# Performance work log

Measured on AMD Instinct MI355X. Metric: run time of the kernel, lower is better.

Reference implementation:

```python
import jax, jax.numpy as jnp
import numpy as np
from jax.scipy.special import logsumexp

ALPHA = 1.0
TOP_K = 128
SK_EPS = 0.001   # sinkhorn entropic epsilon
SK_ITERS = 20    # max_iter (thresh early-exit dropped for jit; 20 fixed iters)
CLIP_MIN = 0.0001


def _cdist(x, y):
    # batched Euclidean distance, safe-sqrt so grad at 0 is 0 (matches torch.cdist subgradient)
    d2 = (jnp.sum(x * x, -1)[..., :, None] + jnp.sum(y * y, -1)[..., None, :]
          - 2.0 * jnp.einsum('bnd,bmd->bnm', x, y))
    d2 = jnp.maximum(d2, 0.0)
    safe = jnp.where(d2 > 0, d2, 1.0)
    return jnp.where(d2 > 0, jnp.sqrt(safe), 0.0)


def _sinkhorn(cost, p, q):
    # log-domain entropic OT with marginals p [B,N], q [B,M]
    logp, logq = jnp.log(p), jnp.log(q)

    def M(u, v):
        return (-cost + u[..., :, None] + v[..., None, :]) / SK_EPS

    def body(carry, _):
        u, v = carry
        u = SK_EPS * (logp - logsumexp(M(u, v), axis=-1)) + u
        v = SK_EPS * (logq - logsumexp(M(u, v), axis=-2)) + v
        return (u, v), None

    u0 = jnp.zeros_like(p)
    v0 = jnp.zeros_like(q)
    (u, v), _ = jax.lax.scan(body, (u0, v0), None, length=SK_ITERS)
    return jnp.exp(M(u, v))  # transport plan gamma [B,N,M]


def setup_inputs() -> dict:
    key = jax.random.key(0)
    ks = jax.random.split(key, 6)
    B, N, M, D = 8, 2048, 2048, 256
    return {
        'src': jax.random.normal(ks[0], (B, N, 3), dtype=jnp.float32),
        'tgt': jax.random.normal(ks[1], (B, M, 3), dtype=jnp.float32),
        'src_feats': jax.random.normal(ks[2], (B, N, D), dtype=jnp.float32),
        'tgt_feats': jax.random.uniform(ks[3], (B, M, D), dtype=jnp.float32),
        'src_o': jax.random.uniform(ks[4], (B, N), dtype=jnp.float32),
        'tgt_o': jax.random.uniform(ks[5], (B, M), dtype=jnp.float32),
    }


def reference(src, tgt, src_feats, tgt_feats, src_o, tgt_o):
    src_pi = src_o / jnp.maximum(jnp.sum(src_o, -1, keepdims=True), CLIP_MIN)
    tgt_pi = tgt_o / jnp.maximum(jnp.sum(tgt_o, -1, keepdims=True), CLIP_MIN)
    cost = _cdist(src_feats, tgt_feats)                       # [B,N,M]
    gamma = _sinkhorn(cost, src_pi, tgt_pi)                   # [B,N,M]
    src_corr = (jnp.einsum('bnm,bmd->bnd', gamma, tgt)
                / jnp.maximum(jnp.sum(gamma, -1, keepdims=True), CLIP_MIN))
    prob = jnp.max(gamma, axis=-1)                            # [B,N]
    _, idx = jax.lax.top_k(prob, TOP_K)                       # [B,K]
    src_k = jnp.take_along_axis(src, idx[:, :, None], axis=1)       # [B,K,3]
    tgt_k = jnp.take_along_axis(src_corr, idx[:, :, None], axis=1)  # [B,K,3]
    alpha2 = ALPHA * ALPHA
    src_edge = _cdist(src_k, src_k)
    tgt_edge = _cdist(tgt_k, tgt_k)
    z = jnp.abs(src_edge - tgt_edge)
    loss = jnp.sum(1.0 - jnp.exp(-0.5 * z * z / alpha2), axis=-1)
    return jnp.mean(loss)
```

## Files before the change

kernel.cpp:

```cpp
#include <hip/hip_runtime.h>
#include <math.h>

#define Bb 8
#define Nn 2048
#define Mm 2048
#define Dd 256
#define TOPK 128
#define SK_ITERS 20
#define RB 8
#define NEG_INIT (-1e30f)
#define SCALE_L2 (-1442.6950408889634f)

__device__ __forceinline__ void lse_merge(float& m, float& s, float m2, float s2) {
    float d = m2 - m;
    float e = exp2f(-fabsf(d));
    bool up = (d > 0.f);
    s = up ? fmaf(s, e, s2) : fmaf(s2, e, s);
    m = up ? m2 : m;
}

__global__ void wl_init_kernel(const float* __restrict__ src_o, const float* __restrict__ tgt_o,
                               float* __restrict__ logp2, float* __restrict__ logq2,
                               float* __restrict__ Ve) {
    __shared__ float lds[8];
    int b = blockIdx.x, t = threadIdx.x;
    int l = t & 63, w = t >> 6;
    float s = 0.f, q = 0.f;
    for (int i = t; i < Nn; i += 256) s += src_o[b * Nn + i];
    for (int i = t; i < Mm; i += 256) q += tgt_o[b * Mm + i];
    for (int o = 32; o; o >>= 1) { s += __shfl_xor(s, o); q += __shfl_xor(q, o); }
    if (l == 0) { lds[w] = s; lds[4 + w] = q; }
    __syncthreads();
    float ssum = fmaxf(lds[0] + lds[1] + lds[2] + lds[3], 1e-4f);
    float qsum = fmaxf(lds[4] + lds[5] + lds[6] + lds[7], 1e-4f);
    float rs = 1.f / ssum, rq = 1.f / qsum;
    for (int i = t; i < Nn; i += 256) logp2[b * Nn + i] = log2f(src_o[b * Nn + i] * rs);
    for (int i = t; i < Mm; i += 256) { logq2[b * Mm + i] = log2f(tgt_o[b * Mm + i] * rq); Ve[b * Mm + i] = 0.f; }
}

__global__ void wl_norms_kernel(const float* __restrict__ feats, float* __restrict__ out) {
    int w = threadIdx.x >> 6, l = threadIdx.x & 63;
    int row = blockIdx.x * 4 + w;
    float4 f = ((const float4*)(feats + (size_t)row * Dd))[l];
    float s = f.x * f.x + f.y * f.y + f.z * f.z + f.w * f.w;
    for (int o = 32; o; o >>= 1) s += __shfl_xor(s, o);
    if (l == 0) out[row] = s;
}

#define BT 128
#define KT 32
#define LDT 132
__global__ __launch_bounds__(256)
void wl_cost_kernel(const float* __restrict__ A, const float* __restrict__ Bf,
                    const float* __restrict__ nx, const float* __restrict__ ny,
                    float* __restrict__ Sc) {
    __shared__ float As[KT][LDT];
    __shared__ float Bs[KT][LDT];
    int b = blockIdx.z;
    int n0 = blockIdx.y * BT, m0 = blockIdx.x * BT;
    const float* Ab = A + (size_t)b * Nn * Dd;
    const float* Bbp = Bf + (size_t)b * Mm * Dd;
    int t = threadIdx.x;
    int w = t >> 6, l = t & 63;
    int tx = (w & 1) * 8 + (l & 7);
    int ty = (w >> 1) * 8 + (l >> 3);
    float acc[8][8] = {};
    for (int k0 = 0; k0 < Dd; k0 += KT) {
        __syncthreads();
#pragma unroll
        for (int i = 0; i < 4; i++) {
            int c = t + 256 * i;
            int row = c >> 3, kc = (c & 7) << 2;
            float4 v = *(const float4*)(Ab + (size_t)(n0 + row) * Dd + k0 + kc);
            As[kc + 0][row] = v.x; As[kc + 1][row] = v.y; As[kc + 2][row] = v.z; As[kc + 3][row] = v.w;
            float4 u = *(const float4*)(Bbp + (size_t)(m0 + row) * Dd + k0 + kc);
            Bs[kc + 0][row] = u.x; Bs[kc + 1][row] = u.y; Bs[kc + 2][row] = u.z; Bs[kc + 3][row] = u.w;
        }
        __syncthreads();
#pragma unroll 4
        for (int k = 0; k < KT; k++) {
            float4 a0 = *(const float4*)&As[k][ty * 8];
            float4 a1 = *(const float4*)&As[k][ty * 8 + 4];
            float4 b0 = *(const float4*)&Bs[k][tx * 8];
            float4 b1 = *(const float4*)&Bs[k][tx * 8 + 4];
            float a[8] = { a0.x, a0.y, a0.z, a0.w, a1.x, a1.y, a1.z, a1.w };
            float bv[8] = { b0.x, b0.y, b0.z, b0.w, b1.x, b1.y, b1.z, b1.w };
#pragma unroll
            for (int i = 0; i < 8; i++)
#pragma unroll
                for (int j = 0; j < 8; j++)
                    acc[i][j] = fmaf(a[i], bv[j], acc[i][j]);
        }
    }
    float nyv[8];
#pragma unroll
    for (int j = 0; j < 8; j++) nyv[j] = ny[b * Mm + m0 + tx * 8 + j];
#pragma unroll
    for (int i = 0; i < 8; i++) {
        int n = n0 + ty * 8 + i;
        float nxv = nx[b * Nn + n];
        float o[8];
#pragma unroll
        for (int j = 0; j < 8; j++) {
            float d2 = nxv + nyv[j] - 2.f * acc[i][j];
            d2 = fmaxf(d2, 0.f);
            float c = d2 > 0.f ? sqrtf(d2) : 0.f;
            o[j] = SCALE_L2 * c;
        }
        float* orow = Sc + ((size_t)b * Nn + n) * Mm + m0 + tx * 8;
        *(float4*)orow = make_float4(o[0], o[1], o[2], o[3]);
        *(float4*)(orow + 4) = make_float4(o[4], o[5], o[6], o[7]);
    }
}

__global__ __launch_bounds__(512)
void wl_fused_kernel(const float* __restrict__ Sc, const float* __restrict__ Ve,
                     const float* __restrict__ logp2, float* __restrict__ Ue,
                     float* __restrict__ pmx, float* __restrict__ psm, int nch) {
    __shared__ float prm[2][RB][8];
    __shared__ float prs[2][RB][8];
    int b = blockIdx.y, ch = blockIdx.x;
    int t = threadIdx.x, w = t >> 6, l = t & 63;
    int chrows = Nn / nch;
    int row0 = ch * chrows;
    int colbase = (w << 8) | (l << 2);

    float4 ve = *(const float4*)(Ve + b * Mm + colbase);
    float cm0 = NEG_INIT, cm1 = NEG_INIT, cm2 = NEG_INIT, cm3 = NEG_INIT;
    float cs0 = 0.f, cs1 = 0.f, cs2 = 0.f, cs3 = 0.f;

    const float* scb = Sc + ((size_t)b * Nn + row0) * Mm + colbase;
    const float* lpb = logp2 + b * Nn + row0;
    float* ueb = Ue + b * Nn + row0;

    for (int r0 = 0; r0 < chrows; r0 += RB) {
        int par = (r0 / RB) & 1;
        float4 tv[RB];
#pragma unroll
        for (int r = 0; r < RB; r++) {
            float4 sv = *(const float4*)(scb + (size_t)(r0 + r) * Mm);
            tv[r].x = sv.x + ve.x; tv[r].y = sv.y + ve.y;
            tv[r].z = sv.z + ve.z; tv[r].w = sv.w + ve.w;
        }
#pragma unroll
        for (int r = 0; r < RB; r++) {
            float m = fmaxf(fmaxf(tv[r].x, tv[r].y), fmaxf(tv[r].z, tv[r].w));
            for (int o = 32; o; o >>= 1) m = fmaxf(m, __shfl_xor(m, o));
            float s = exp2f(tv[r].x - m) + exp2f(tv[r].y - m)
                    + exp2f(tv[r].z - m) + exp2f(tv[r].w - m);
            for (int o = 32; o; o >>= 1) s += __shfl_xor(s, o);
            if (l == 0) { prm[par][r][w] = m; prs[par][r][w] = s; }
        }
        __syncthreads();
#pragma unroll
        for (int r = 0; r < RB; r++) {
            float M = prm[par][r][0];
#pragma unroll
            for (int ww = 1; ww < 8; ww++) M = fmaxf(M, prm[par][r][ww]);
            float S = 0.f;
#pragma unroll
            for (int ww = 0; ww < 8; ww++) S = fmaf(prs[par][r][ww], exp2f(prm[par][r][ww] - M), S);
            float C = lpb[r0 + r] - log2f(S) - M;
            if (t == 0) ueb[r0 + r] = C;
            lse_merge(cm0, cs0, tv[r].x + C, 1.f);
            lse_merge(cm1, cs1, tv[r].y + C, 1.f);
            lse_merge(cm2, cs2, tv[r].z + C, 1.f);
            lse_merge(cm3, cs3, tv[r].w + C, 1.f);
        }
    }
    size_t gi = ((size_t)(b * nch + ch)) * Mm + colbase;
    *(float4*)(pmx + gi) = make_float4(cm0, cm1, cm2, cm3);
    *(float4*)(psm + gi) = make_float4(cs0, cs1, cs2, cs3);
}

__global__ void wl_v_combine_kernel(const float* __restrict__ pmx, const float* __restrict__ psm,
                                    const float* __restrict__ logq2, float* __restrict__ Ve, int nch) {
    int idx = blockIdx.x * 256 + threadIdx.x;
    int b = idx >> 11, m = idx & (Mm - 1);
    const float* pbm = pmx + (size_t)b * nch * Mm + m;
    const float* pbs = psm + (size_t)b * nch * Mm + m;
    float m0 = NEG_INIT, s0 = 0.f, m1 = NEG_INIT, s1 = 0.f;
    float m2 = NEG_INIT, s2 = 0.f, m3 = NEG_INIT, s3 = 0.f;
    for (int ch = 0; ch < nch; ch += 4) {
        lse_merge(m0, s0, pbm[(size_t)(ch + 0) * Mm], pbs[(size_t)(ch + 0) * Mm]);
        lse_merge(m1, s1, pbm[(size_t)(ch + 1) * Mm], pbs[(size_t)(ch + 1) * Mm]);
        lse_merge(m2, s2, pbm[(size_t)(ch + 2) * Mm], pbs[(size_t)(ch + 2) * Mm]);
        lse_merge(m3, s3, pbm[(size_t)(ch + 3) * Mm], pbs[(size_t)(ch + 3) * Mm]);
    }
    lse_merge(m0, s0, m1, s1);
    lse_merge(m2, s2, m3, s3);
    lse_merge(m0, s0, m2, s2);
    Ve[idx] = logq2[idx] + Ve[idx] - m0 - log2f(s0);
}

__global__ __launch_bounds__(256)
void wl_finalize_kernel(const float* __restrict__ Sc, const float* __restrict__ Ue,
                        const float* __restrict__ Ve, const float* __restrict__ tgt,
                        float* __restrict__ prob, float* __restrict__ corr) {
    int w = threadIdx.x >> 6, l = threadIdx.x & 63;
    int row = blockIdx.x * 4 + w;
    int b = row >> 11;
    const float4* s4 = (const float4*)(Sc + (size_t)row * Mm);
    const float4* v4 = (const float4*)(Ve + (size_t)b * Mm);
    const float4* tg4 = (const float4*)(tgt + (size_t)b * Mm * 3);
    float mx = NEG_INIT, sm = 0.f, w0 = 0.f, w1 = 0.f, w2 = 0.f;
#pragma unroll
    for (int i = 0; i < 8; i++) {
        int c = l + 64 * i;
        float4 sv = s4[c]; float4 vv = v4[c];
        float4 g0 = tg4[3 * c + 0], g1 = tg4[3 * c + 1], g2 = tg4[3 * c + 2];
        float tt[4] = { sv.x + vv.x, sv.y + vv.y, sv.z + vv.z, sv.w + vv.w };
        float gx[4] = { g0.x, g0.w, g1.z, g2.y };
        float gy[4] = { g0.y, g1.x, g1.w, g2.z };
        float gz[4] = { g0.z, g1.y, g2.x, g2.w };
#pragma unroll
        for (int j = 0; j < 4; j++) {
            float nm = fmaxf(mx, tt[j]);
            float ce = exp2f(mx - nm), e = exp2f(tt[j] - nm);
            sm = sm * ce + e;
            w0 = w0 * ce + e * gx[j];
            w1 = w1 * ce + e * gy[j];
            w2 = w2 * ce + e * gz[j];
            mx = nm;
        }
    }
    for (int o = 32; o; o >>= 1) {
        float om = __shfl_xor(mx, o), os = __shfl_xor(sm, o);
        float o0 = __shfl_xor(w0, o), o1 = __shfl_xor(w1, o), o2 = __shfl_xor(w2, o);
        float nm = fmaxf(mx, om);
        float c1 = exp2f(mx - nm), c2 = exp2f(om - nm);
        sm = sm * c1 + os * c2;
        w0 = w0 * c1 + o0 * c2;
        w1 = w1 * c1 + o1 * c2;
        w2 = w2 * c1 + o2 * c2;
        mx = nm;
    }
    if (l == 0) {
        float scale = exp2f(Ue[row] + mx);
        float rowsum = scale * sm;
        float den = fmaxf(rowsum, 1e-4f);
        prob[row] = scale;
        corr[(size_t)row * 3 + 0] = scale * w0 / den;
        corr[(size_t)row * 3 + 1] = scale * w1 / den;
        corr[(size_t)row * 3 + 2] = scale * w2 / den;
    }
}

__global__ __launch_bounds__(256)
void wl_topk_kernel(const float* __restrict__ prob, int* __restrict__ topk) {
    __shared__ float key[2048];
    __shared__ int val[2048];
    int b = blockIdx.x, t = threadIdx.x;
    for (int i = t; i < 2048; i += 256) { key[i] = prob[b * 2048 + i]; val[i] = i; }
    __syncthreads();
    for (int size = 2; size <= 2048; size <<= 1) {
        for (int stride = size >> 1; stride > 0; stride >>= 1) {
            for (int q = t; q < 1024; q += 256) {
                int i = 2 * q - (q & (stride - 1));
                int j = i + stride;
                bool up = ((i & size) == 0);
                float ki = key[i], kj = key[j];
                int vi = val[i], vj = val[j];
                bool jBetter = (kj > ki) || (kj == ki && vj < vi);
                if (up ? jBetter : !jBetter) {
                    key[i] = kj; key[j] = ki;
                    val[i] = vj; val[j] = vi;
                }
            }
            __syncthreads();
        }
    }
    if (t < TOPK) topk[b * TOPK + t] = val[t];
}

__global__ __launch_bounds__(256)
void wl_edge_kernel(const float* __restrict__ src, const float* __restrict__ corr,
                    const int* __restrict__ topk, float* __restrict__ bloss) {
    __shared__ float sx[TOPK][3];
    __shared__ float tx[TOPK][3];
    __shared__ float lds[4];
    int b = blockIdx.x, t = threadIdx.x;
    if (t < TOPK) {
        int id = topk[b * TOPK + t];
        sx[t][0] = src[((size_t)b * 2048 + id) * 3 + 0];
        sx[t][1] = src[((size_t)b * 2048 + id) * 3 + 1];
        sx[t][2] = src[((size_t)b * 2048 + id) * 3 + 2];
        tx[t][0] = corr[((size_t)b * 2048 + id) * 3 + 0];
        tx[t][1] = corr[((size_t)b * 2048 + id) * 3 + 1];
        tx[t][2] = corr[((size_t)b * 2048 + id) * 3 + 2];
    }
    __syncthreads();
    float acc = 0.f;
    for (int p = t; p < TOPK * TOPK; p += 256) {
        int i = p >> 7, j = p & 127;
        float dx = sx[i][0] - sx[j][0], dy = sx[i][1] - sx[j][1], dz = sx[i][2] - sx[j][2];
        float d2s = dx * dx + dy * dy + dz * dz;
        float ds = d2s > 0.f ? sqrtf(d2s) : 0.f;
        float ex = tx[i][0] - tx[j][0], ey = tx[i][1] - tx[j][1], ez = tx[i][2] - tx[j][2];
        float d2t = ex * ex + ey * ey + ez * ez;
        float dt = d2t > 0.f ? sqrtf(d2t) : 0.f;
        float z = fabsf(ds - dt);
        acc += 1.f - expf(-0.5f * z * z);
    }
    int l = t & 63, w = t >> 6;
    for (int o = 32; o; o >>= 1) acc += __shfl_xor(acc, o);
    if (l == 0) lds[w] = acc;
    __syncthreads();
    if (t == 0) bloss[b] = lds[0] + lds[1] + lds[2] + lds[3];
}

__global__ void wl_final_kernel(const float* __restrict__ bloss, float* __restrict__ out) {
    if (threadIdx.x == 0) {
        float s = 0.f;
        for (int i = 0; i < Bb; i++) s += bloss[i];
        out[0] = s / 1024.f;
    }
}

extern "C" void kernel_launch(void* const* d_in, const int* in_sizes, int n_in,
                              void* d_out, int out_size, void* d_ws, size_t ws_size,
                              hipStream_t stream) {
    (void)in_sizes; (void)n_in; (void)out_size;
    const float* src       = (const float*)d_in[0];
    const float* tgt       = (const float*)d_in[1];
    const float* src_feats = (const float*)d_in[2];
    const float* tgt_feats = (const float*)d_in[3];
    const float* src_o     = (const float*)d_in[4];
    const float* tgt_o     = (const float*)d_in[5];
    float* out = (float*)d_out;

    size_t fixed = (size_t)Bb * Nn * Mm + 7 * (size_t)Bb * Nn + 3 * (size_t)Bb * Nn
                 + (size_t)Bb * TOPK + Bb + 64;
    int nch = (ws_size >= (fixed + 2 * (size_t)Bb * 64 * Mm) * sizeof(float)) ? 64 : 32;

    float* ws = (float*)d_ws;
    size_t off = 0;
    float* Sc    = ws + off; off += (size_t)Bb * Nn * Mm;
    float* Ue    = ws + off; off += Bb * Nn;
    float* Ve    = ws + off; off += Bb * Mm;
    float* logp2 = ws + off; off += Bb * Nn;
    float* logq2 = ws + off; off += Bb * Mm;
    float* nx    = ws + off; off += Bb * Nn;
    float* ny    = ws + off; off += Bb * Mm;
    float* prob  = ws + off; off += Bb * Nn;
    float* corr  = ws + off; off += (size_t)Bb * Nn * 3;
    float* pmx   = ws + off; off += (size_t)Bb * nch * Mm;
    float* psm   = ws + off; off += (size_t)Bb * nch * Mm;
    int*   topk  = (int*)(ws + off); off += Bb * TOPK;
    float* bloss = ws + off; off += Bb;
    if (ws_size < off * sizeof(float)) return;

    wl_init_kernel<<<Bb, 256, 0, stream>>>(src_o, tgt_o, logp2, logq2, Ve);
    wl_norms_kernel<<<(Bb * Nn) / 4, 256, 0, stream>>>(src_feats, nx);
    wl_norms_kernel<<<(Bb * Mm) / 4, 256, 0, stream>>>(tgt_feats, ny);
    wl_cost_kernel<<<dim3(Mm / BT, Nn / BT, Bb), 256, 0, stream>>>(src_feats, tgt_feats, nx, ny, Sc);

    for (int it = 0; it < SK_ITERS; it++) {
        wl_fused_kernel<<<dim3(nch, Bb), 512, 0, stream>>>(Sc, Ve, logp2, Ue, pmx, psm, nch);
        wl_v_combine_kernel<<<(Bb * Mm) / 256, 256, 0, stream>>>(pmx, psm, logq2, Ve, nch);
    }

    wl_finalize_kernel<<<(Bb * Nn) / 4, 256, 0, stream>>>(Sc, Ue, Ve, tgt, prob, corr);
    wl_topk_kernel<<<Bb, 256, 0, stream>>>(prob, topk);
    wl_edge_kernel<<<Bb, 256, 0, stream>>>(src, corr, topk, bloss);
    wl_final_kernel<<<1, 64, 0, stream>>>(bloss, out);
}
```

Baseline: 1.699 ms.

## Double-buffer Sinkhorn row loads, split combine across chunk quarters, widen top-k sort

The fused Sinkhorn row kernel now prefetches the next batch of cost rows into a second register buffer while the current batch is reduced, so global load latency overlaps with the exp and shuffle work. The column combine kernel splits the chunk-partial merge across four thread groups and finishes the merge through shared memory, which launches more blocks and shortens each thread's serial chain. The bitonic top-k runs with 1024 threads, one compare-swap per thread per stage. Costs: the doubled register buffers may lower occupancy, and an odd batch count relies on the clamped extra load and redundant processing.

```diff
diff --git a/kernel.cpp b/kernel.cpp
--- a/kernel.cpp
+++ b/kernel.cpp
@@ -113,6 +113,50 @@
     }
 }
 
+__device__ __forceinline__ void wl_load_batch(float4 (&tv)[RB], const float* scb,
+                                              int batch, int nbatch, float4 ve) {
+    int rr = batch < nbatch ? batch : nbatch - 1;
+    const float* p = scb + (size_t)rr * RB * Mm;
+#pragma unroll
+    for (int r = 0; r < RB; r++) {
+        float4 sv = *(const float4*)(p + (size_t)r * Mm);
+        tv[r].x = sv.x + ve.x; tv[r].y = sv.y + ve.y;
+        tv[r].z = sv.z + ve.z; tv[r].w = sv.w + ve.w;
+    }
+}
+
+__device__ __forceinline__ void wl_proc_batch(float4 (&tv)[RB], int par, int rbase,
+        float (&prm)[2][RB][8], float (&prs)[2][RB][8],
+        const float* lpb, float* ueb, int t, int w, int l,
+        float& cm0, float& cs0, float& cm1, float& cs1,
+        float& cm2, float& cs2, float& cm3, float& cs3) {
+#pragma unroll
+    for (int r = 0; r < RB; r++) {
+        float m = fmaxf(fmaxf(tv[r].x, tv[r].y), fmaxf(tv[r].z, tv[r].w));
+        for (int o = 32; o; o >>= 1) m = fmaxf(m, __shfl_xor(m, o));
+        float s = exp2f(tv[r].x - m) + exp2f(tv[r].y - m)
+                + exp2f(tv[r].z - m) + exp2f(tv[r].w - m);
+        for (int o = 32; o; o >>= 1) s += __shfl_xor(s, o);
+        if (l == 0) { prm[par][r][w] = m; prs[par][r][w] = s; }
+    }
+    __syncthreads();
+#pragma unroll
+    for (int r = 0; r < RB; r++) {
+        float M = prm[par][r][0];
+#pragma unroll
+        for (int ww = 1; ww < 8; ww++) M = fmaxf(M, prm[par][r][ww]);
+        float S = 0.f;
+#pragma unroll
+        for (int ww = 0; ww < 8; ww++) S = fmaf(prs[par][r][ww], exp2f(prm[par][r][ww] - M), S);
+        float C = lpb[rbase + r] - log2f(S) - M;
+        if (t == 0) ueb[rbase + r] = C;
+        lse_merge(cm0, cs0, tv[r].x + C, 1.f);
+        lse_merge(cm1, cs1, tv[r].y + C, 1.f);
+        lse_merge(cm2, cs2, tv[r].z + C, 1.f);
+        lse_merge(cm3, cs3, tv[r].w + C, 1.f);
+    }
+}
+
 __global__ __launch_bounds__(512)
 void wl_fused_kernel(const float* __restrict__ Sc, const float* __restrict__ Ve,
                      const float* __restrict__ logp2, float* __restrict__ Ue,
@@ -133,64 +177,44 @@
     const float* lpb = logp2 + b * Nn + row0;
     float* ueb = Ue + b * Nn + row0;
 
-    for (int r0 = 0; r0 < chrows; r0 += RB) {
-        int par = (r0 / RB) & 1;
-        float4 tv[RB];
-#pragma unroll
-        for (int r = 0; r < RB; r++) {
-            float4 sv = *(const float4*)(scb + (size_t)(r0 + r) * Mm);
-            tv[r].x = sv.x + ve.x; tv[r].y = sv.y + ve.y;
-            tv[r].z = sv.z + ve.z; tv[r].w = sv.w + ve.w;
-        }
-#pragma unroll
-        for (int r = 0; r < RB; r++) {
-            float m = fmaxf(fmaxf(tv[r].x, tv[r].y), fmaxf(tv[r].z, tv[r].w));
-            for (int o = 32; o; o >>= 1) m = fmaxf(m, __shfl_xor(m, o));
-            float s = exp2f(tv[r].x - m) + exp2f(tv[r].y - m)
-                    + exp2f(tv[r].z - m) + exp2f(tv[r].w - m);
-            for (int o = 32; o; o >>= 1) s += __shfl_xor(s, o);
-            if (l == 0) { prm[par][r][w] = m; prs[par][r][w] = s; }
-        }
-        __syncthreads();
-#pragma unroll
-        for (int r = 0; r < RB; r++) {
-            float M = prm[par][r][0];
-#pragma unroll
-            for (int ww = 1; ww < 8; ww++) M = fmaxf(M, prm[par][r][ww]);
-            float S = 0.f;
-#pragma unroll
-            for (int ww = 0; ww < 8; ww++) S = fmaf(prs[par][r][ww], exp2f(prm[par][r][ww] - M), S);
-            float C = lpb[r0 + r] - log2f(S) - M;
-            if (t == 0) ueb[r0 + r] = C;
-            lse_merge(cm0, cs0, tv[r].x + C, 1.f);
-            lse_merge(cm1, cs1, tv[r].y + C, 1.f);
-            lse_merge(cm2, cs2, tv[r].z + C, 1.f);
-            lse_merge(cm3, cs3, tv[r].w + C, 1.f);
-        }
-    }
+    int nbatch = chrows / RB;
+    float4 tva[RB], tvb[RB];
+    wl_load_batch(tva, scb, 0, nbatch, ve);
+    for (int i = 0; i < nbatch; i += 2) {
+        wl_load_batch(tvb, scb, i + 1, nbatch, ve);
+        wl_proc_batch(tva, 0, i * RB, prm, prs, lpb, ueb, t, w, l,
+                      cm0, cs0, cm1, cs1, cm2, cs2, cm3, cs3);
+        wl_load_batch(tva, scb, i + 2, nbatch, ve);
+        wl_proc_batch(tvb, 1, (i + 1) * RB, prm, prs, lpb, ueb, t, w, l,
+                      cm0, cs0, cm1, cs1, cm2, cs2, cm3, cs3);
+    }
+
     size_t gi = ((size_t)(b * nch + ch)) * Mm + colbase;
     *(float4*)(pmx + gi) = make_float4(cm0, cm1, cm2, cm3);
     *(float4*)(psm + gi) = make_float4(cs0, cs1, cs2, cs3);
 }
 
-__global__ void wl_v_combine_kernel(const float* __restrict__ pmx, const float* __restrict__ psm,
-                                    const float* __restrict__ logq2, float* __restrict__ Ve, int nch) {
-    int idx = blockIdx.x * 256 + threadIdx.x;
-    int b = idx >> 11, m = idx & (Mm - 1);
-    const float* pbm = pmx + (size_t)b * nch * Mm + m;
-    const float* pbs = psm + (size_t)b * nch * Mm + m;
-    float m0 = NEG_INIT, s0 = 0.f, m1 = NEG_INIT, s1 = 0.f;
-    float m2 = NEG_INIT, s2 = 0.f, m3 = NEG_INIT, s3 = 0.f;
-    for (int ch = 0; ch < nch; ch += 4) {
-        lse_merge(m0, s0, pbm[(size_t)(ch + 0) * Mm], pbs[(size_t)(ch + 0) * Mm]);
-        lse_merge(m1, s1, pbm[(size_t)(ch + 1) * Mm], pbs[(size_t)(ch + 1) * Mm]);
-        lse_merge(m2, s2, pbm[(size_t)(ch + 2) * Mm], pbs[(size_t)(ch + 2) * Mm]);
-        lse_merge(m3, s3, pbm[(size_t)(ch + 3) * Mm], pbs[(size_t)(ch + 3) * Mm]);
-    }
-    lse_merge(m0, s0, m1, s1);
-    lse_merge(m2, s2, m3, s3);
-    lse_merge(m0, s0, m2, s2);
-    Ve[idx] = logq2[idx] + Ve[idx] - m0 - log2f(s0);
+__global__ __launch_bounds__(256)
+void wl_v_combine_kernel(const float* __restrict__ pmx, const float* __restrict__ psm,
+                         const float* __restrict__ logq2, float* __restrict__ Ve, int nch) {
+    __shared__ float lm[4][64], ls[4][64];
+    int t = threadIdx.x;
+    int quarter = t >> 6, cidx = t & 63;
+    int col = blockIdx.x * 64 + cidx;
+    int b = col >> 11, m = col & (Mm - 1);
+    int cpq = nch >> 2;
+    const float* pbm = pmx + ((size_t)(b * nch + quarter * cpq)) * Mm + m;
+    const float* pbs = psm + ((size_t)(b * nch + quarter * cpq)) * Mm + m;
+    float mx = NEG_INIT, sm = 0.f;
+    for (int ch = 0; ch < cpq; ch++)
+        lse_merge(mx, sm, pbm[(size_t)ch * Mm], pbs[(size_t)ch * Mm]);
+    lm[quarter][cidx] = mx; ls[quarter][cidx] = sm;
+    __syncthreads();
+    if (quarter == 0) {
+#pragma unroll
+        for (int qq = 1; qq < 4; qq++) lse_merge(mx, sm, lm[qq][cidx], ls[qq][cidx]);
+        Ve[col] = logq2[col] + Ve[col] - mx - log2f(sm);
+    }
 }
 
 __global__ __launch_bounds__(256)
@@ -246,26 +270,25 @@
     }
 }
 
-__global__ __launch_bounds__(256)
+__global__ __launch_bounds__(1024)
 void wl_topk_kernel(const float* __restrict__ prob, int* __restrict__ topk) {
     __shared__ float key[2048];
     __shared__ int val[2048];
     int b = blockIdx.x, t = threadIdx.x;
-    for (int i = t; i < 2048; i += 256) { key[i] = prob[b * 2048 + i]; val[i] = i; }
+    for (int i = t; i < 2048; i += 1024) { key[i] = prob[b * 2048 + i]; val[i] = i; }
     __syncthreads();
     for (int size = 2; size <= 2048; size <<= 1) {
         for (int stride = size >> 1; stride > 0; stride >>= 1) {
-            for (int q = t; q < 1024; q += 256) {
-                int i = 2 * q - (q & (stride - 1));
-                int j = i + stride;
-                bool up = ((i & size) == 0);
-                float ki = key[i], kj = key[j];
-                int vi = val[i], vj = val[j];
-                bool jBetter = (kj > ki) || (kj == ki && vj < vi);
-                if (up ? jBetter : !jBetter) {
-                    key[i] = kj; key[j] = ki;
-                    val[i] = vj; val[j] = vi;
-                }
+            int q = t;
+            int i = 2 * q - (q & (stride - 1));
+            int j = i + stride;
+            bool up = ((i & size) == 0);
+            float ki = key[i], kj = key[j];
+            int vi = val[i], vj = val[j];
+            bool jBetter = (kj > ki) || (kj == ki && vj < vi);
+            if (up ? jBetter : !jBetter) {
+                key[i] = kj; key[j] = ki;
+                val[i] = vj; val[j] = vi;
             }
             __syncthreads();
         }
@@ -357,11 +380,11 @@
 
     for (int it = 0; it < SK_ITERS; it++) {
         wl_fused_kernel<<<dim3(nch, Bb), 512, 0, stream>>>(Sc, Ve, logp2, Ue, pmx, psm, nch);
-        wl_v_combine_kernel<<<(Bb * Mm) / 256, 256, 0, stream>>>(pmx, psm, logq2, Ve, nch);
+        wl_v_combine_kernel<<<(Bb * Mm) / 64, 256, 0, stream>>>(pmx, psm, logq2, Ve, nch);
     }
 
     wl_finalize_kernel<<<(Bb * Nn) / 4, 256, 0, stream>>>(Sc, Ue, Ve, tgt, prob, corr);
-    wl_topk_kernel<<<Bb, 256, 0, stream>>>(prob, topk);
+    wl_topk_kernel<<<Bb, 1024, 0, stream>>>(prob, topk);
     wl_edge_kernel<<<Bb, 256, 0, stream>>>(src, corr, topk, bloss);
     wl_final_kernel<<<1, 64, 0, stream>>>(bloss, out);
 }
```

After: 1.992 ms. +17.2%, slower.
